# Kernel tuning notes

Hardware: AMD Instinct MI355X
Metric: run time of the kernel (lower is better)

The kernel has to match this reference:

```python
import jax, jax.numpy as jnp
import numpy as np

NUM_HEADS, HEAD_DIM = 4, 64
BLOCK_SIZE, S = 32, 4
LENGTHS = np.array([2048, 1024, 1536, 512, 2048, 1280, 1792, 768])
MAX_LEN = int(LENGTHS.max())            # 2048
NUM_BLOCKS = MAX_LEN // BLOCK_SIZE      # 64
B = len(LENGTHS)
T = int(LENGTHS.sum())                  # 11008
HIDDEN = NUM_HEADS * HEAD_DIM           # 256
SCALE = HEAD_DIM ** -0.5
INV_SCALE = 1.0 / SCALE
EPS = 1e-6


def setup_inputs() -> dict:
    key = jax.random.key(0)
    ks = jax.random.split(key, 6)
    offsets = np.concatenate([[0], np.cumsum(LENGTHS)]).astype(np.int64)
    batch_ids = np.repeat(np.arange(B), LENGTHS).astype(np.int64)
    pos_ids = np.concatenate([np.arange(l) for l in LENGTHS]).astype(np.int64)
    shp = (T, NUM_HEADS, HEAD_DIM)
    return {
        "q": jax.random.normal(ks[0], shp, jnp.float32),
        "k": jax.random.normal(ks[1], shp, jnp.float32),
        "v": jax.random.normal(ks[2], shp, jnp.float32),
        "u": jax.random.normal(ks[3], shp, jnp.float32),
        "Wg_cmp": jax.random.normal(ks[4], (NUM_HEADS, HEAD_DIM), jnp.float32) * 0.1,
        "Wg_slc": jax.random.normal(ks[5], (NUM_HEADS, HEAD_DIM), jnp.float32) * 0.1,
        "x_offsets": jnp.asarray(offsets),
        "batch_ids": jnp.asarray(batch_ids),
        "pos_ids": jnp.asarray(pos_ids),
    }


def _silu(x):
    return x * jax.nn.sigmoid(x)


def _layer_norm(x):
    # non-affine LayerNorm over last dim, eps=1e-6
    mu = jnp.mean(x, -1, keepdims=True)
    var = jnp.mean(jnp.square(x - mu), -1, keepdims=True)
    return (x - mu) / jnp.sqrt(var + EPS)


def _forward(q, k, v, u, Wg_cmp, Wg_slc, x_offsets, batch_ids, pos_ids):
    # jagged -> padded dense [B, MAX_LEN, H, D]
    pad = lambda x: jnp.zeros((B, MAX_LEN, NUM_HEADS, HEAD_DIM), x.dtype).at[batch_ids, pos_ids].set(x)
    pq, pk, pv = pad(q), pad(k), pad(v)

    # gate model: per-head sigmoid linear gates from padded_q; g_slc is unused
    # by the original forward (the slc kernel never consumes it)
    g_cmp = jax.nn.sigmoid(jnp.einsum('bnhd,hd->bnh', pq, Wg_cmp))
    _g_slc = jax.nn.sigmoid(jnp.einsum('bnhd,hd->bnh', pq, Wg_slc))
    g_cmp_jag = g_cmp[batch_ids, pos_ids]  # [T, H]

    # block-compressed K/V: mean over zero-padded blocks of size BLOCK_SIZE
    k_cmp = pk.reshape(B, NUM_BLOCKS, BLOCK_SIZE, NUM_HEADS, HEAD_DIM).mean(2)
    v_cmp = pv.reshape(B, NUM_BLOCKS, BLOCK_SIZE, NUM_HEADS, HEAD_DIM).mean(2)

    # SiLU-activated block-causal compressed attention
    raw = jnp.einsum('bnhd,bmhd->bnhm', pq, k_cmp) * SCALE  # [B, n, H, m]
    q_blk = jnp.arange(MAX_LEN) // BLOCK_SIZE
    k_blk = jnp.arange(NUM_BLOCKS)
    causal = q_blk[:, None] >= k_blk[None, :]   # [MAX_LEN, NUM_BLOCKS]
    local = q_blk[:, None] == k_blk[None, :]
    p_cmp = jnp.where(causal[None, :, None, :], _silu(raw) * INV_SCALE, 0.0)

    # top-S block selection; local block score forced to 1.0; odd slots
    # duplicated from even slots (as in source)
    sel = jnp.where(local[None, :, None, :], 1.0, p_cmp)
    topk = jax.lax.top_k(sel, S)[1]             # [B, MAX_LEN, H, S]
    topk = topk.at[..., 1::2].set(topk[..., 0::2])
    topk_jag = topk[batch_ids, pos_ids]         # [T, H, S]

    # compressed-branch output, gathered to jagged and gated by g_cmp
    o_cmp = jnp.einsum('bnhm,bmhd->bnhd', p_cmp, v_cmp)[batch_ids, pos_ids]
    o_cmp = o_cmp * g_cmp_jag[:, :, None]       # [T, H, D]

    # selected branch: per-row, per-head gather of S blocks of raw K/V
    seq_start = x_offsets[batch_ids]            # [T]
    head_ix = jnp.arange(NUM_HEADS)[None, :, None]
    o_slc = jnp.zeros_like(q)
    for s in range(S):  # fixed small S, duplicates intentionally double-count
        b_idx = topk_jag[:, :, s]               # [T, H]
        pos_in_seq = b_idx[:, :, None] * BLOCK_SIZE + jnp.arange(BLOCK_SIZE)  # [T,H,BS]
        valid = (b_idx[:, :, None] >= 0) & (pos_in_seq <= pos_ids[:, None, None])
        tgt = jnp.clip(seq_start[:, None, None] + pos_in_seq, 0, T - 1)
        k_g = k[tgt, head_ix]                   # [T, H, BS, D]
        score = jnp.einsum('thd,thbd->thb', q, k_g) * SCALE
        p = jnp.where(valid, _silu(score) * INV_SCALE, 0.0)
        v_g = v[tgt, head_ix]                   # [T, H, BS, D]
        o_slc = o_slc + jnp.einsum('thb,thbd->thd', p, v_g)

    # per-token LayerNorm over hidden, scaled by u, then branch sum
    o_cmp = _layer_norm(o_cmp.reshape(T, HIDDEN)).reshape(T, NUM_HEADS, HEAD_DIM) * u
    o_slc = _layer_norm(o_slc.reshape(T, HIDDEN)).reshape(T, NUM_HEADS, HEAD_DIM) * u
    return (o_cmp + o_slc).reshape(T, HIDDEN)


def reference(q, k, v, u, Wg_cmp, Wg_slc, x_offsets, batch_ids, pos_ids):
    return _forward(q, k, v, u, Wg_cmp, Wg_slc, x_offsets, batch_ids, pos_ids)
```

## Files before the change

kernel.cpp:

```cpp
#include <hip/hip_runtime.h>
#include <math.h>

#define NH 4
#define HD 64
#define HIDDEN 256
#define BS 32
#define NB 64
#define SCALE 0.125f
#define INV_SCALE 8.0f

__device__ __forceinline__ float fast_sigmoid(float x) {
    return 1.0f / (1.0f + __expf(-x));
}
__device__ __forceinline__ float readlane_f(float v, int lane) {
    return __int_as_float(__builtin_amdgcn_readlane(__float_as_int(v), lane));
}

__global__ __launch_bounds__(256) void kcmp_kernel(
    const float* __restrict__ k, const float* __restrict__ v,
    const int* __restrict__ x_offsets,
    double* __restrict__ k_cmp, float* __restrict__ v_cmp2) {
    int bb  = blockIdx.x;
    int b   = bb >> 6;
    int blk = bb & 63;
    int tid = threadIdx.x;
    int s0   = x_offsets[b];
    int len  = x_offsets[b + 1] - s0;
    int nblk = len >> 5;
    int h = tid >> 6, d = tid & 63;
    if (blockIdx.y == 0) {
        double acc = 0.0;
        if (blk < nblk) {
            const float* kp = k + (size_t)(s0 + blk * BS) * HIDDEN + tid;
            #pragma unroll
            for (int i = 0; i < BS; ++i) acc += (double)kp[i * HIDDEN];
            acc *= (1.0 / BS);
        }
        k_cmp[((size_t)(b * NH + h) * 64 + blk) * 64 + d] = acc;
    } else {
        float acc = 0.f;
        if (blk < nblk) {
            const float* vp = v + (size_t)(s0 + blk * BS) * HIDDEN + tid;
            #pragma unroll
            for (int i = 0; i < BS; ++i) acc += vp[i * HIDDEN];
            acc *= (1.0f / BS);
        }
        v_cmp2[((size_t)(b * NH + h) * 32 + (blk >> 1)) * 128 + d * 2 + (blk & 1)] = acc;
    }
}

__global__ __launch_bounds__(256, 3) void cmp_kernel(
    const float* __restrict__ q,
    const int* __restrict__ batch_ids, const int* __restrict__ pos_ids,
    const double* __restrict__ k_cmp, const float* __restrict__ v_cmp2,
    float* __restrict__ oc_buf, int2* __restrict__ idxbuf, int T) {
    int t0   = blockIdx.x * 64;
    int h    = blockIdx.y;
    int tid  = threadIdx.x;
    int wv   = __builtin_amdgcn_readfirstlane(tid >> 6);
    int lane = tid & 63;
    int b    = batch_ids[t0];
    int pos0 = pos_ids[t0];

    __shared__ __align__(16) char smem[49920];
    float* qs = (float*)smem;
    float* ps = qs + 64 * 65;
    float* vs = ps + 64 * 66;
    unsigned long long* trip = (unsigned long long*)qs;

    const float* qg = q + (size_t)t0 * HIDDEN + h * HD;
    #pragma unroll
    for (int i = 0; i < 16; ++i) {
        int idx = tid + 256 * i;
        int tok = idx >> 6, dd = idx & 63;
        qs[dd * 65 + tok] = qg[(size_t)tok * HIDDEN + dd];
    }
    const float* vg = v_cmp2 + (size_t)(b * NH + h) * 4096;
    #pragma unroll
    for (int i = 0; i < 16; ++i) vs[tid + 256 * i] = vg[tid + 256 * i];
    __syncthreads();

    int qblk_max = (pos0 + 63) >> 5;
    int m_need   = qblk_max + 2;
    if (m_need > 63) m_need = 63;

    unsigned long long a0 = 0ull, a1 = 0ull, a2 = 0ull;
    if (16 * wv <= m_need) {
        double qd[64];
        #pragma unroll
        for (int dd = 0; dd < 64; ++dd) qd[dd] = (double)qs[dd * 65 + lane];
        int myqblk = (pos0 + lane) >> 5;

        const double* kcb = k_cmp + ((size_t)(b * NH + h) * 64 + wv * 16) * 64;
        #pragma unroll
        for (int mi = 0; mi < 16; ++mi) {
            int m = wv * 16 + mi;
            const double* kr = kcb + mi * 64;
            double accA = 0.0, accB = 0.0;
            #pragma unroll
            for (int dd = 0; dd < 32; ++dd) {
                accA += qd[2 * dd]     * kr[2 * dd];
                accB += qd[2 * dd + 1] * kr[2 * dd + 1];
            }
            double r = (accA + accB) * 0.125;
            double p64 = 0.0;
            if (m <= myqblk) p64 = r / (1.0 + exp(-r)) * 8.0;
            double selv = (m == myqblk) ? 1.0 : p64;
            ps[lane * 66 + m] = (float)p64;
            long long sb = __double_as_longlong(selv);
            unsigned long long kk = (unsigned long long)sb;
            kk = (sb < 0) ? ~kk : (kk | 0x8000000000000000ull);
            kk = (kk & ~63ull) | (unsigned long long)(63 - m);
            if (kk > a0)      { a2 = a1; a1 = a0; a0 = kk; }
            else if (kk > a1) { a2 = a1; a1 = kk; }
            else if (kk > a2) { a2 = kk; }
        }
    }
    __syncthreads();
    trip[(wv * 64 + lane) * 3 + 0] = a0;
    trip[(wv * 64 + lane) * 3 + 1] = a1;
    trip[(wv * 64 + lane) * 3 + 2] = a2;
    __syncthreads();

    if (wv == 0) {
        unsigned long long kk2[4][3];
        #pragma unroll
        for (int w = 0; w < 4; ++w)
            #pragma unroll
            for (int j = 0; j < 3; ++j)
                kk2[w][j] = trip[(w * 64 + lane) * 3 + j];
        int pp[4] = {0, 0, 0, 0};
        int outi[3];
        #pragma unroll
        for (int s = 0; s < 3; ++s) {
            unsigned long long best = 0ull; int bw = 0;
            #pragma unroll
            for (int w = 0; w < 4; ++w) {
                unsigned long long hd_ = (pp[w] == 0) ? kk2[w][0]
                                       : (pp[w] == 1) ? kk2[w][1] : kk2[w][2];
                if (hd_ > best) { best = hd_; bw = w; }
            }
            outi[s] = 63 - (int)(best & 63ull);
            #pragma unroll
            for (int w = 0; w < 4; ++w) if (w == bw) pp[w]++;
        }
        idxbuf[(size_t)(t0 + lane) * NH + h] = make_int2(outi[0], outi[2]);
    }

    float occ[16];
    #pragma unroll
    for (int tt = 0; tt < 16; ++tt) occ[tt] = 0.f;
    int mmax2 = qblk_max >> 1;
    const float2* vs2 = (const float2*)vs;
    for (int m2 = 0; m2 <= mmax2; ++m2) {
        float2 vv = vs2[m2 * 64 + lane];
        #pragma unroll
        for (int tt = 0; tt < 16; ++tt) {
            int tok = wv * 16 + tt;
            float2 pv = *(const float2*)(ps + tok * 66 + 2 * m2);
            occ[tt] += pv.x * vv.x + pv.y * vv.y;
        }
    }
    #pragma unroll
    for (int tt = 0; tt < 16; ++tt)
        oc_buf[(size_t)(t0 + wv * 16 + tt) * HIDDEN + h * HD + lane] = occ[tt];
}

__global__ __launch_bounds__(256, 8) void hstu_main_kernel(
    const float* __restrict__ q, const float* __restrict__ k,
    const float* __restrict__ v, const float* __restrict__ u,
    const float* __restrict__ Wg_cmp,
    const int* __restrict__ x_offsets, const int* __restrict__ batch_ids,
    const int* __restrict__ pos_ids,
    const float* __restrict__ oc_buf, const int2* __restrict__ idxbuf,
    float* __restrict__ out, int T) {
    int i   = blockIdx.x;
    int t   = ((T & 7) == 0) ? ((i & 7) * (T >> 3) + (i >> 3)) : i;
    int tid = threadIdx.x;
    int h = __builtin_amdgcn_readfirstlane(tid >> 6);
    int d = tid & 63;
    int b    = batch_ids[t];
    int pos  = pos_ids[t];
    int s0   = x_offsets[b];
    int qblk = pos >> 5;

    int2 ix  = idxbuf[(size_t)t * NH + h];
    int idx0 = ix.x, idx2 = ix.y;

    const float* qrow = q + (size_t)t * HIDDEN + h * HD;
    float qv = qrow[d];

    float gsum = qv * Wg_cmp[h * HD + d];
    #pragma unroll
    for (int off = 32; off; off >>= 1) gsum += __shfl_xor(gsum, off, 64);
    float g = fast_sigmoid(gsum);

    float oc = oc_buf[(size_t)t * HIDDEN + tid] * g;

    int r = d & 15, c = d >> 4;
    float4 qf[4];
    {
        const float4* q4 = (const float4*)qrow;
        #pragma unroll
        for (int j = 0; j < 4; ++j) qf[j] = q4[c + 4 * j];
    }
    float pl[4];
    #pragma unroll
    for (int it = 0; it < 4; ++it) {
        int blk_l = (it >= 2) ? idx2 : idx0;
        int ii    = (it & 1) * 16 + r;
        int pis   = blk_l * BS + ii;
        int tgt   = s0 + pis;
        if (tgt > T - 1) tgt = T - 1;
        const float4* kr = (const float4*)(k + (size_t)tgt * HIDDEN + h * HD) + c;
        float psum = 0.f;
        #pragma unroll
        for (int j = 0; j < 4; ++j) {
            float4 kk = kr[j * 4];
            psum += qf[j].x * kk.x + qf[j].y * kk.y + qf[j].z * kk.z + qf[j].w * kk.w;
        }
        psum += __shfl_xor(psum, 16, 64);
        psum += __shfl_xor(psum, 32, 64);
        float scv = psum * SCALE;
        pl[it] = (pis <= pos) ? scv * fast_sigmoid(scv) * (INV_SCALE * 2.0f) : 0.f;
    }

    int bsafe1 = (idx2 > qblk) ? 0 : idx2;
    const float* vr0 = v + (size_t)(s0 + idx0  * BS) * HIDDEN + h * HD + d;
    const float* vr1 = v + (size_t)(s0 + bsafe1 * BS) * HIDDEN + h * HD + d;
    float os0 = 0.f, os1 = 0.f, os2 = 0.f, os3 = 0.f;
    #pragma unroll
    for (int i2 = 0; i2 < 16; ++i2) {
        os0 += readlane_f(pl[0], i2) * vr0[i2 * HIDDEN];
        os1 += readlane_f(pl[1], i2) * vr0[(16 + i2) * HIDDEN];
        os2 += readlane_f(pl[2], i2) * vr1[i2 * HIDDEN];
        os3 += readlane_f(pl[3], i2) * vr1[(16 + i2) * HIDDEN];
    }
    float os = (os0 + os1) + (os2 + os3);

    __shared__ float red[NH][4];
    float sc_ = oc, sc2 = oc * oc, ss_ = os, ss2 = os * os;
    #pragma unroll
    for (int off = 32; off; off >>= 1) {
        sc_ += __shfl_xor(sc_, off, 64);
        sc2 += __shfl_xor(sc2, off, 64);
        ss_ += __shfl_xor(ss_, off, 64);
        ss2 += __shfl_xor(ss2, off, 64);
    }
    if (d == 0) { red[h][0] = sc_; red[h][1] = sc2; red[h][2] = ss_; red[h][3] = ss2; }
    __syncthreads();
    float tc = 0.f, tc2 = 0.f, ts = 0.f, ts2 = 0.f;
    #pragma unroll
    for (int w = 0; w < NH; ++w) {
        tc += red[w][0]; tc2 += red[w][1]; ts += red[w][2]; ts2 += red[w][3];
    }
    float muc  = tc  * (1.0f / HIDDEN);
    float varc = tc2 * (1.0f / HIDDEN) - muc * muc;
    float mus  = ts  * (1.0f / HIDDEN);
    float vars = ts2 * (1.0f / HIDDEN) - mus * mus;
    float uval = u[(size_t)t * HIDDEN + tid];
    float outv = (oc - muc) * rsqrtf(varc + 1e-6f) * uval
               + (os - mus) * rsqrtf(vars + 1e-6f) * uval;
    out[(size_t)t * HIDDEN + tid] = outv;
}

extern "C" void kernel_launch(void* const* d_in, const int* in_sizes, int n_in,
                              void* d_out, int out_size, void* d_ws, size_t ws_size,
                              hipStream_t stream) {
    const float* q      = (const float*)d_in[0];
    const float* k      = (const float*)d_in[1];
    const float* v      = (const float*)d_in[2];
    const float* u      = (const float*)d_in[3];
    const float* Wg_cmp = (const float*)d_in[4];
    const int* x_offsets = (const int*)d_in[6];
    const int* batch_ids = (const int*)d_in[7];
    const int* pos_ids   = (const int*)d_in[8];

    int T = in_sizes[0] / HIDDEN;
    int B = in_sizes[6] - 1;

    double* k_cmp  = (double*)d_ws;
    float*  v_cmp2 = (float*)(k_cmp + (size_t)B * NH * 4096);
    float*  oc_buf = v_cmp2 + (size_t)B * NH * 4096;
    int2*   idxbuf = (int2*)(oc_buf + (size_t)T * HIDDEN);

    kcmp_kernel<<<dim3(B * NB, 2), 256, 0, stream>>>(k, v, x_offsets, k_cmp, v_cmp2);
    cmp_kernel<<<dim3(T / 64, NH), 256, 0, stream>>>(
        q, batch_ids, pos_ids, k_cmp, v_cmp2, oc_buf, idxbuf, T);
    hstu_main_kernel<<<T, 256, 0, stream>>>(q, k, v, u, Wg_cmp,
                                            x_offsets, batch_ids, pos_ids,
                                            oc_buf, idxbuf, (float*)d_out, T);
}
```

Baseline: 241.4 us.

## Split selection attention into per-query-block kernel with shared K/V block reuse

Replaces the per-token fused main kernel with two kernels. The first processes 32 query tokens per head per wavefront: it takes the union of the selected key blocks, loads each K/V block once into registers, and serves every token that selected it, so K/V gathers are shared across tokens. A separate vectorized LayerNorm/gating kernel then combines the compressed branch with the selection result, writing in place to the output. This cuts redundant global K/V reads, at the cost of an extra launch, an intermediate round trip through the output buffer, and serialized per-token work inside a wavefront.

```diff
diff --git a/kernel.cpp b/kernel.cpp
--- a/kernel.cpp
+++ b/kernel.cpp
@@ -166,102 +166,163 @@
         oc_buf[(size_t)(t0 + wv * 16 + tt) * HIDDEN + h * HD + lane] = occ[tt];
 }
 
-__global__ __launch_bounds__(256, 8) void hstu_main_kernel(
+__global__ __launch_bounds__(64) void slc_kernel(
     const float* __restrict__ q, const float* __restrict__ k,
-    const float* __restrict__ v, const float* __restrict__ u,
-    const float* __restrict__ Wg_cmp,
+    const float* __restrict__ v,
     const int* __restrict__ x_offsets, const int* __restrict__ batch_ids,
     const int* __restrict__ pos_ids,
-    const float* __restrict__ oc_buf, const int2* __restrict__ idxbuf,
-    float* __restrict__ out, int T) {
-    int i   = blockIdx.x;
-    int t   = ((T & 7) == 0) ? ((i & 7) * (T >> 3) + (i >> 3)) : i;
+    const int2* __restrict__ idxbuf, float* __restrict__ os_out, int T) {
+    int i  = blockIdx.x;
+    int wg = (i & 7) * (gridDim.x >> 3) + (i >> 3);
+    int qb = wg >> 2;
+    int h  = wg & 3;
+    int t0 = qb * 32;
+    int lane = threadIdx.x;
+
+    int b    = batch_ids[t0];
+    int pos0 = pos_ids[t0];
+    int s0   = x_offsets[b];
+    int qblk = pos0 >> 5;
+
+    __shared__ float q_lds[32 * 68];
+    __shared__ float os_lds[32 * 64];
+
+    const float4* q4 = (const float4*)(q + (size_t)t0 * HIDDEN + h * HD);
+    #pragma unroll
+    for (int rep = 0; rep < 8; ++rep) {
+        int f4i = lane + 64 * rep;
+        int tk = f4i >> 4, c4 = f4i & 15;
+        *(float4*)(&q_lds[tk * 68 + c4 * 4]) = q4[(size_t)tk * 64 + c4];
+    }
+    #pragma unroll
+    for (int rep = 0; rep < 32; ++rep) os_lds[lane + 64 * rep] = 0.f;
+
+    int myi0 = -1, myi2 = -1;
+    unsigned long long U = 0ull;
+    if (lane < 32) {
+        int2 ix = idxbuf[(size_t)(t0 + lane) * NH + h];
+        myi0 = ix.x;
+        myi2 = (ix.y <= qblk) ? ix.y : -1;
+        U = (1ull << myi0);
+        if (myi2 >= 0) U |= (1ull << myi2);
+    }
+    #pragma unroll
+    for (int off = 1; off < 64; off <<= 1) U |= __shfl_xor(U, off, 64);
+
+    int r  = lane & 15, cc = lane >> 4;
+    const float* kbase = k + (size_t)s0 * HIDDEN + h * HD;
+    const float* vbase = v + (size_t)s0 * HIDDEN + h * HD + lane;
+
+    while (U) {
+        int m = (int)__builtin_ctzll(U); U &= U - 1;
+        const float* kb_p = kbase + (size_t)(m * BS) * HIDDEN;
+        float4 kb0[4], kb1[4];
+        #pragma unroll
+        for (int j = 0; j < 4; ++j) {
+            kb0[j] = *(const float4*)(kb_p + (size_t)r * HIDDEN + (cc + 4 * j) * 4);
+            kb1[j] = *(const float4*)(kb_p + (size_t)(16 + r) * HIDDEN + (cc + 4 * j) * 4);
+        }
+        float vb[32];
+        const float* vb_p = vbase + (size_t)(m * BS) * HIDDEN;
+        #pragma unroll
+        for (int row = 0; row < 32; ++row) vb[row] = vb_p[(size_t)row * HIDDEN];
+
+        unsigned long long want =
+            __ballot(lane < 32 && (myi0 == m || myi2 == m));
+        while (want) {
+            int tk = (int)__builtin_ctzll(want); want &= want - 1;
+            int pos_tk = pos0 + tk;
+            const float* qrow = &q_lds[tk * 68];
+            float psum0 = 0.f, psum1 = 0.f;
+            #pragma unroll
+            for (int j = 0; j < 4; ++j) {
+                float4 qq = *(const float4*)(qrow + (cc + 4 * j) * 4);
+                psum0 += qq.x * kb0[j].x + qq.y * kb0[j].y
+                       + qq.z * kb0[j].z + qq.w * kb0[j].w;
+                psum1 += qq.x * kb1[j].x + qq.y * kb1[j].y
+                       + qq.z * kb1[j].z + qq.w * kb1[j].w;
+            }
+            psum0 += __shfl_xor(psum0, 16, 64); psum0 += __shfl_xor(psum0, 32, 64);
+            psum1 += __shfl_xor(psum1, 16, 64); psum1 += __shfl_xor(psum1, 32, 64);
+            float scv0 = psum0 * SCALE, scv1 = psum1 * SCALE;
+            int row0 = m * BS + r;
+            float p0 = (row0 <= pos_tk)      ? scv0 * fast_sigmoid(scv0) * 16.f : 0.f;
+            float p1 = (row0 + 16 <= pos_tk) ? scv1 * fast_sigmoid(scv1) * 16.f : 0.f;
+            float ost = 0.f;
+            #pragma unroll
+            for (int rr = 0; rr < 16; ++rr) {
+                ost += readlane_f(p0, rr) * vb[rr];
+                ost += readlane_f(p1, rr) * vb[16 + rr];
+            }
+            os_lds[tk * 64 + lane] += ost;
+        }
+    }
+
+    float* ob = os_out + (size_t)t0 * HIDDEN + h * HD + lane;
+    #pragma unroll
+    for (int tk = 0; tk < 32; ++tk)
+        ob[(size_t)tk * HIDDEN] = os_lds[tk * 64 + lane];
+}
+
+__global__ __launch_bounds__(256) void ln_kernel(
+    const float* __restrict__ q, const float* __restrict__ u,
+    const float* __restrict__ Wg_cmp,
+    const float* __restrict__ oc_buf, float* __restrict__ io, int T) {
     int tid = threadIdx.x;
-    int h = __builtin_amdgcn_readfirstlane(tid >> 6);
-    int d = tid & 63;
-    int b    = batch_ids[t];
-    int pos  = pos_ids[t];
-    int s0   = x_offsets[b];
-    int qblk = pos >> 5;
-
-    int2 ix  = idxbuf[(size_t)t * NH + h];
-    int idx0 = ix.x, idx2 = ix.y;
-
-    const float* qrow = q + (size_t)t * HIDDEN + h * HD;
-    float qv = qrow[d];
-
-    float gsum = qv * Wg_cmp[h * HD + d];
-    #pragma unroll
-    for (int off = 32; off; off >>= 1) gsum += __shfl_xor(gsum, off, 64);
-    float g = fast_sigmoid(gsum);
-
-    float oc = oc_buf[(size_t)t * HIDDEN + tid] * g;
-
-    int r = d & 15, c = d >> 4;
-    float4 qf[4];
-    {
-        const float4* q4 = (const float4*)qrow;
-        #pragma unroll
-        for (int j = 0; j < 4; ++j) qf[j] = q4[c + 4 * j];
-    }
-    float pl[4];
-    #pragma unroll
-    for (int it = 0; it < 4; ++it) {
-        int blk_l = (it >= 2) ? idx2 : idx0;
-        int ii    = (it & 1) * 16 + r;
-        int pis   = blk_l * BS + ii;
-        int tgt   = s0 + pis;
-        if (tgt > T - 1) tgt = T - 1;
-        const float4* kr = (const float4*)(k + (size_t)tgt * HIDDEN + h * HD) + c;
-        float psum = 0.f;
-        #pragma unroll
-        for (int j = 0; j < 4; ++j) {
-            float4 kk = kr[j * 4];
-            psum += qf[j].x * kk.x + qf[j].y * kk.y + qf[j].z * kk.z + qf[j].w * kk.w;
-        }
-        psum += __shfl_xor(psum, 16, 64);
-        psum += __shfl_xor(psum, 32, 64);
-        float scv = psum * SCALE;
-        pl[it] = (pis <= pos) ? scv * fast_sigmoid(scv) * (INV_SCALE * 2.0f) : 0.f;
-    }
-
-    int bsafe1 = (idx2 > qblk) ? 0 : idx2;
-    const float* vr0 = v + (size_t)(s0 + idx0  * BS) * HIDDEN + h * HD + d;
-    const float* vr1 = v + (size_t)(s0 + bsafe1 * BS) * HIDDEN + h * HD + d;
-    float os0 = 0.f, os1 = 0.f, os2 = 0.f, os3 = 0.f;
-    #pragma unroll
-    for (int i2 = 0; i2 < 16; ++i2) {
-        os0 += readlane_f(pl[0], i2) * vr0[i2 * HIDDEN];
-        os1 += readlane_f(pl[1], i2) * vr0[(16 + i2) * HIDDEN];
-        os2 += readlane_f(pl[2], i2) * vr1[i2 * HIDDEN];
-        os3 += readlane_f(pl[3], i2) * vr1[(16 + i2) * HIDDEN];
-    }
-    float os = (os0 + os1) + (os2 + os3);
-
-    __shared__ float red[NH][4];
-    float sc_ = oc, sc2 = oc * oc, ss_ = os, ss2 = os * os;
-    #pragma unroll
-    for (int off = 32; off; off >>= 1) {
+    int grp = tid >> 5;
+    int sub = tid & 31;
+    int t   = blockIdx.x * 8 + grp;
+    int D0  = sub * 8;
+
+    const float4* qp = (const float4*)(q + (size_t)t * HIDDEN + D0);
+    float4 qa = qp[0], qb = qp[1];
+    const float4* wp = (const float4*)(Wg_cmp + D0);
+    float4 wa = wp[0], wb = wp[1];
+    float gp = qa.x * wa.x + qa.y * wa.y + qa.z * wa.z + qa.w * wa.w
+             + qb.x * wb.x + qb.y * wb.y + qb.z * wb.z + qb.w * wb.w;
+    gp += __shfl_xor(gp, 1, 64);
+    gp += __shfl_xor(gp, 2, 64);
+    gp += __shfl_xor(gp, 4, 64);
+    float g = fast_sigmoid(gp);
+
+    const float4* ocp = (const float4*)(oc_buf + (size_t)t * HIDDEN + D0);
+    float4 oa = ocp[0], ob = ocp[1];
+    oa.x *= g; oa.y *= g; oa.z *= g; oa.w *= g;
+    ob.x *= g; ob.y *= g; ob.z *= g; ob.w *= g;
+    float4* iop = (float4*)(io + (size_t)t * HIDDEN + D0);
+    float4 sa = iop[0], sb = iop[1];
+
+    float sc_ = oa.x + oa.y + oa.z + oa.w + ob.x + ob.y + ob.z + ob.w;
+    float sc2 = oa.x * oa.x + oa.y * oa.y + oa.z * oa.z + oa.w * oa.w
+              + ob.x * ob.x + ob.y * ob.y + ob.z * ob.z + ob.w * ob.w;
+    float ss_ = sa.x + sa.y + sa.z + sa.w + sb.x + sb.y + sb.z + sb.w;
+    float ss2 = sa.x * sa.x + sa.y * sa.y + sa.z * sa.z + sa.w * sa.w
+              + sb.x * sb.x + sb.y * sb.y + sb.z * sb.z + sb.w * sb.w;
+    #pragma unroll
+    for (int off = 1; off < 32; off <<= 1) {
         sc_ += __shfl_xor(sc_, off, 64);
         sc2 += __shfl_xor(sc2, off, 64);
         ss_ += __shfl_xor(ss_, off, 64);
         ss2 += __shfl_xor(ss2, off, 64);
     }
-    if (d == 0) { red[h][0] = sc_; red[h][1] = sc2; red[h][2] = ss_; red[h][3] = ss2; }
-    __syncthreads();
-    float tc = 0.f, tc2 = 0.f, ts = 0.f, ts2 = 0.f;
-    #pragma unroll
-    for (int w = 0; w < NH; ++w) {
-        tc += red[w][0]; tc2 += red[w][1]; ts += red[w][2]; ts2 += red[w][3];
-    }
-    float muc  = tc  * (1.0f / HIDDEN);
-    float varc = tc2 * (1.0f / HIDDEN) - muc * muc;
-    float mus  = ts  * (1.0f / HIDDEN);
-    float vars = ts2 * (1.0f / HIDDEN) - mus * mus;
-    float uval = u[(size_t)t * HIDDEN + tid];
-    float outv = (oc - muc) * rsqrtf(varc + 1e-6f) * uval
-               + (os - mus) * rsqrtf(vars + 1e-6f) * uval;
-    out[(size_t)t * HIDDEN + tid] = outv;
+    float muc  = sc_ * (1.0f / HIDDEN);
+    float varc = sc2 * (1.0f / HIDDEN) - muc * muc;
+    float mus  = ss_ * (1.0f / HIDDEN);
+    float vars = ss2 * (1.0f / HIDDEN) - mus * mus;
+    float rc = rsqrtf(varc + 1e-6f), rs = rsqrtf(vars + 1e-6f);
+
+    const float4* up = (const float4*)(u + (size_t)t * HIDDEN + D0);
+    float4 ua = up[0], ub = up[1];
+    float4 o0, o1;
+    o0.x = ((oa.x - muc) * rc + (sa.x - mus) * rs) * ua.x;
+    o0.y = ((oa.y - muc) * rc + (sa.y - mus) * rs) * ua.y;
+    o0.z = ((oa.z - muc) * rc + (sa.z - mus) * rs) * ua.z;
+    o0.w = ((oa.w - muc) * rc + (sa.w - mus) * rs) * ua.w;
+    o1.x = ((ob.x - muc) * rc + (sb.x - mus) * rs) * ub.x;
+    o1.y = ((ob.y - muc) * rc + (sb.y - mus) * rs) * ub.y;
+    o1.z = ((ob.z - muc) * rc + (sb.z - mus) * rs) * ub.z;
+    o1.w = ((ob.w - muc) * rc + (sb.w - mus) * rs) * ub.w;
+    iop[0] = o0; iop[1] = o1;
 }
 
 extern "C" void kernel_launch(void* const* d_in, const int* in_sizes, int n_in,
@@ -287,7 +348,8 @@
     kcmp_kernel<<<dim3(B * NB, 2), 256, 0, stream>>>(k, v, x_offsets, k_cmp, v_cmp2);
     cmp_kernel<<<dim3(T / 64, NH), 256, 0, stream>>>(
         q, batch_ids, pos_ids, k_cmp, v_cmp2, oc_buf, idxbuf, T);
-    hstu_main_kernel<<<T, 256, 0, stream>>>(q, k, v, u, Wg_cmp,
-                                            x_offsets, batch_ids, pos_ids,
-                                            oc_buf, idxbuf, (float*)d_out, T);
-}
+    slc_kernel<<<dim3((T / 32) * NH), 64, 0, stream>>>(
+        q, k, v, x_offsets, batch_ids, pos_ids, idxbuf, (float*)d_out, T);
+    ln_kernel<<<dim3(T / 8), 256, 0, stream>>>(
+        q, u, Wg_cmp, oc_buf, (float*)d_out, T);
+}
```

After: 206.3 us. 14.6% less time.
